# Kernel optimization log

Measured on AMD Instinct MI355X. Metric: run time of the kernel, lower is better.

The kernel has to match this reference:

```python
import jax, jax.numpy as jnp
import numpy as np

B = 65536
IN_F = 1024
OUT_F = 1024
N_ACT = 4  # len(activation_functions): tanh, sin, relu, sigmoid (cyclic over columns)


def setup_inputs() -> dict:
    key = jax.random.key(0)
    k1, k2 = jax.random.split(key)
    x = jax.random.normal(k1, (B, IN_F), dtype=jnp.float32)
    # xavier_uniform for weight [out, in]
    limit = float(np.sqrt(6.0 / (IN_F + OUT_F)))
    W = jax.random.uniform(k2, (OUT_F, IN_F), dtype=jnp.float32, minval=-limit, maxval=limit)
    b = jnp.zeros((OUT_F,), dtype=jnp.float32)
    return {"input": x, "W": W, "b": b}


def _apply_cyclic_acts(y):
    # column i gets activation (i % N_ACT); OUT_F % N_ACT == 0 so reshape to groups
    Bb, O = y.shape
    yg = y.reshape(Bb, O // N_ACT, N_ACT)
    out = jnp.stack([
        jnp.tanh(yg[..., 0]),
        jnp.sin(yg[..., 1]),
        jax.nn.relu(yg[..., 2]),
        jax.nn.sigmoid(yg[..., 3]),
    ], axis=-1)
    return out.reshape(Bb, O)


def reference(input, W, b) -> jnp.ndarray:
    y = jnp.einsum('bi,oi->bo', input, W) + b  # F.linear
    return _apply_cyclic_acts(y)
```

## Files before the change

### kernel.cpp

```cpp
#include <hip/hip_runtime.h>

constexpr int B_ROWS = 65536;
constexpr int IN_F   = 1024;
constexpr int OUT_F  = 1024;

constexpr int BDIM = 512;
constexpr int BM = 256, BN = 256, BK = 64;

typedef __bf16 bf16x8 __attribute__((ext_vector_type(8)));
typedef float  f32x4  __attribute__((ext_vector_type(4)));

__device__ __forceinline__ bf16x8 cvt8(f32x4 u0, f32x4 u1) {
    bf16x8 v;
    v[0] = (__bf16)u0[0]; v[1] = (__bf16)u0[1]; v[2] = (__bf16)u0[2]; v[3] = (__bf16)u0[3];
    v[4] = (__bf16)u1[0]; v[5] = (__bf16)u1[1]; v[6] = (__bf16)u1[2]; v[7] = (__bf16)u1[3];
    return v;
}

__device__ __forceinline__ void glds16(const __bf16* g, unsigned char* l) {
    __builtin_amdgcn_global_load_lds(
        (const __attribute__((address_space(1))) unsigned int*)(const void*)g,
        (__attribute__((address_space(3))) unsigned int*)(void*)l,
        16, 0, 0);
}

__global__ __launch_bounds__(256)
void w_to_bf16(const float* __restrict__ W, __bf16* __restrict__ Wb) {
    const size_t i = ((size_t)blockIdx.x * 256 + threadIdx.x) * 16;
    f32x4 a0 = *(const f32x4*)(W + i);
    f32x4 a1 = *(const f32x4*)(W + i + 4);
    f32x4 a2 = *(const f32x4*)(W + i + 8);
    f32x4 a3 = *(const f32x4*)(W + i + 12);
    *(bf16x8*)(Wb + i)     = cvt8(a0, a1);
    *(bf16x8*)(Wb + i + 8) = cvt8(a2, a3);
}

__global__ __launch_bounds__(BDIM, 2)
void fused_linear_act(const float* __restrict__ X,
                      const __bf16* __restrict__ Wb,
                      const float* __restrict__ bias,
                      float* __restrict__ O)
{
    __shared__ __attribute__((aligned(16))) unsigned char lds[2 * 65536];

    const int bx  = blockIdx.x;
    const int xcd = bx & 7;
    const int idx = bx >> 3;
    const int nt  = idx & 3;
    const int mt  = xcd + 8 * (idx >> 2);
    const int m0 = mt * BM;
    const int n0 = nt * BN;

    const int tid  = threadIdx.x;
    const int lane = tid & 63;
    const int wave = tid >> 6;
    const int wr2  = wave >> 2;
    const int w4   = wave & 3;
    const int lrow = lane & 15;
    const int quad = lane >> 4;

    const int arow = tid >> 1;
    const int ah   = tid & 1;
    const float* asrc = X + (size_t)(m0 + arow) * IN_F + ah * 32;
    const int awr = ah * 16384 + (arow >> 4) * 1024 + (arow & 15) * 16;

    const __bf16* bgp = Wb + (size_t)(n0 + 32 * wave + lrow) * IN_F + quad * 8;

    unsigned char* const b0 = lds;
    unsigned char* const b1 = lds + 65536;

    f32x4 acc[8][4];
    #pragma unroll
    for (int i = 0; i < 8; ++i)
        #pragma unroll
        for (int j = 0; j < 4; ++j)
            acc[i][j] = (f32x4){0.f, 0.f, 0.f, 0.f};

    f32x4 ar0, ar1, ar2, ar3, ar4, ar5, ar6, ar7;
    bf16x8 aq0, aq1, aq2, aq3, bq0, bq1, bq2, bq3;

#define ALOAD_LO(KA) do { \
    ar0 = *(const f32x4*)(asrc + (KA));      ar1 = *(const f32x4*)(asrc + (KA) + 4);  \
    ar2 = *(const f32x4*)(asrc + (KA) + 8);  ar3 = *(const f32x4*)(asrc + (KA) + 12); } while (0)
#define ALOAD_HI(KA) do { \
    ar4 = *(const f32x4*)(asrc + (KA) + 16); ar5 = *(const f32x4*)(asrc + (KA) + 20); \
    ar6 = *(const f32x4*)(asrc + (KA) + 24); ar7 = *(const f32x4*)(asrc + (KA) + 28); } while (0)
#define DSW(BUF) do { unsigned char* _w = (BUF) + awr; \
    *(bf16x8*)(_w)       = cvt8(ar0, ar1); \
    *(bf16x8*)(_w + 256) = cvt8(ar2, ar3); \
    *(bf16x8*)(_w + 512) = cvt8(ar4, ar5); \
    *(bf16x8*)(_w + 768) = cvt8(ar6, ar7); } while (0)
#define GBALL(BUF, K) do { unsigned char* _d0 = (BUF) + 32768 + wave * 2048; \
    unsigned char* _d1 = _d0 + 16384; \
    glds16(bgp + (K), _d0);      glds16(bgp + (K) + 16 * IN_F, _d0 + 1024); \
    glds16(bgp + (K) + 32, _d1); glds16(bgp + (K) + 32 + 16 * IN_F, _d1 + 1024); } while (0)
#define RA(BUF, KH, MH) do { \
    const unsigned char* _r = (BUF) + (KH) * 16384 + (wr2 * 8 + (MH) * 4) * 1024 + lane * 16; \
    aq0 = *(const bf16x8*)(_r);        aq1 = *(const bf16x8*)(_r + 1024); \
    aq2 = *(const bf16x8*)(_r + 2048); aq3 = *(const bf16x8*)(_r + 3072); } while (0)
#define RB(BUF, KH) do { \
    const unsigned char* _r = (BUF) + 32768 + (KH) * 16384 + (w4 * 4) * 1024 + lane * 16; \
    bq0 = *(const bf16x8*)(_r);        bq1 = *(const bf16x8*)(_r + 1024); \
    bq2 = *(const bf16x8*)(_r + 2048); bq3 = *(const bf16x8*)(_r + 3072); } while (0)
#define MFMA1(MH, I, J) acc[(MH)*4+(I)][(J)] = \
    __builtin_amdgcn_mfma_f32_16x16x32_bf16(aq##I, bq##J, acc[(MH)*4+(I)][(J)], 0, 0, 0)
#define MFMAQ(MH) do { __builtin_amdgcn_s_setprio(1); \
    MFMA1(MH,0,0); MFMA1(MH,0,1); MFMA1(MH,0,2); MFMA1(MH,0,3); \
    MFMA1(MH,1,0); MFMA1(MH,1,1); MFMA1(MH,1,2); MFMA1(MH,1,3); \
    MFMA1(MH,2,0); MFMA1(MH,2,1); MFMA1(MH,2,2); MFMA1(MH,2,3); \
    MFMA1(MH,3,0); MFMA1(MH,3,1); MFMA1(MH,3,2); MFMA1(MH,3,3); \
    __builtin_amdgcn_s_setprio(0); } while (0)
#define BAR() __builtin_amdgcn_s_barrier()
#define VM8() asm volatile("s_waitcnt vmcnt(8)" ::: "memory")
#define VM0() asm volatile("s_waitcnt vmcnt(0)" ::: "memory")
#define VMNONE() ((void)0)

#define ROUND(CUR, OPP, DO_STAGE, KB1, DO_ALOAD, KA2, VMW) do { \
     if (DO_STAGE) { GBALL(OPP, KB1); DSW(OPP); } \
             RB(CUR, 0); RA(CUR, 0, 0); BAR(); MFMAQ(0); BAR(); \
     if (DO_ALOAD) ALOAD_LO(KA2); \
             RA(CUR, 0, 1); BAR(); MFMAQ(1); BAR(); \
     if (DO_ALOAD) ALOAD_HI(KA2); \
             RB(CUR, 1); RA(CUR, 1, 0); BAR(); MFMAQ(0); BAR(); \
     RA(CUR, 1, 1); BAR(); MFMAQ(1); VMW(); BAR(); \
} while (0)

    ALOAD_LO(0); ALOAD_HI(0);
    GBALL(b0, 0);
    DSW(b0);
    ALOAD_LO(64); ALOAD_HI(64);
    asm volatile("s_waitcnt vmcnt(8) lgkmcnt(0)" ::: "memory");
    BAR();

    #pragma unroll 1
    for (int t = 0; t < 14; t += 2) {
        ROUND(b0, b1, true, (t + 1) * 64, true, (t + 2) * 64, VM8);
        ROUND(b1, b0, true, (t + 2) * 64, true, (t + 3) * 64, VM8);
    }
    ROUND(b0, b1, true, 15 * 64, false, 0, VM0);
    ROUND(b1, b0, false, 0, false, 0, VMNONE);

    const int s = lane & 3;
    const float kmul = (s == 0) ? -2.f : -1.f;
    const float aa   = (s == 0) ?  2.f :  1.f;
    const float cc   = (s == 0) ? -1.f :  0.f;
    const bool  is_sin  = (s == 1);
    const bool  is_relu = (s == 2);

    float bv[4];
    #pragma unroll
    for (int fn = 0; fn < 4; ++fn) bv[fn] = bias[n0 + w4 * 64 + fn * 16 + lrow];

    #pragma unroll
    for (int fm = 0; fm < 8; ++fm) {
        #pragma unroll
        for (int r = 0; r < 4; ++r) {
            const int gr = m0 + wr2 * 128 + fm * 16 + quad * 4 + r;
            float* op = O + (size_t)gr * OUT_F + n0 + w4 * 64 + lrow;
            #pragma unroll
            for (int fn = 0; fn < 4; ++fn) {
                const float y = acc[fm][fn][r] + bv[fn];
                const float e = __expf(kmul * y);
                const float g = fmaf(aa, __builtin_amdgcn_rcpf(1.f + e), cc);
                const float sv = __sinf(y);
                const float rv = fmaxf(y, 0.f);
                const float res = is_sin ? sv : (is_relu ? rv : g);
                op[fn * 16] = res;
            }
        }
    }
}

extern "C" void kernel_launch(void* const* d_in, const int* in_sizes, int n_in,
                              void* d_out, int out_size, void* d_ws, size_t ws_size,
                              hipStream_t stream) {
    const float* X = (const float*)d_in[0];
    const float* W = (const float*)d_in[1];
    const float* b = (const float*)d_in[2];
    float* O = (float*)d_out;
    __bf16* Wb = (__bf16*)d_ws;

    const size_t nW = (size_t)OUT_F * IN_F;
    w_to_bf16<<<(int)(nW / (256 * 16)), 256, 0, stream>>>(W, Wb);

    const int grid = (B_ROWS / BM) * (OUT_F / BN);
    fused_linear_act<<<grid, BDIM, 0, stream>>>(X, Wb, b, O);
}
```

Measured before the change: 613.8 us.

## Split batch between fused fp32-A kernel and pre-converted bf16 GEMM

The first half of the rows is processed by the fused kernel, which loads fp32 X and converts it in registers. This version issues the A loads all at once behind a sched barrier. The second half of X is first converted to bf16 by a separate kernel. That half then runs through a GEMM that streams both A and B via direct global-to-LDS loads, with finer-grained prefetch. The aim is to lower register and VALU pressure and improve load pipelining for part of the batch, at the cost of an extra pass over half of X and extra workspace. If the workspace is too small, the code falls back to the fused-only kernel.

```diff
diff --git a/kernel.cpp b/kernel.cpp
--- a/kernel.cpp
+++ b/kernel.cpp
@@ -35,65 +35,17 @@
     *(bf16x8*)(Wb + i + 8) = cvt8(a2, a3);
 }
 
-__global__ __launch_bounds__(BDIM, 2)
-void fused_linear_act(const float* __restrict__ X,
-                      const __bf16* __restrict__ Wb,
-                      const float* __restrict__ bias,
-                      float* __restrict__ O)
-{
-    __shared__ __attribute__((aligned(16))) unsigned char lds[2 * 65536];
-
-    const int bx  = blockIdx.x;
-    const int xcd = bx & 7;
-    const int idx = bx >> 3;
-    const int nt  = idx & 3;
-    const int mt  = xcd + 8 * (idx >> 2);
-    const int m0 = mt * BM;
-    const int n0 = nt * BN;
-
-    const int tid  = threadIdx.x;
-    const int lane = tid & 63;
-    const int wave = tid >> 6;
-    const int wr2  = wave >> 2;
-    const int w4   = wave & 3;
-    const int lrow = lane & 15;
-    const int quad = lane >> 4;
-
-    const int arow = tid >> 1;
-    const int ah   = tid & 1;
-    const float* asrc = X + (size_t)(m0 + arow) * IN_F + ah * 32;
-    const int awr = ah * 16384 + (arow >> 4) * 1024 + (arow & 15) * 16;
-
-    const __bf16* bgp = Wb + (size_t)(n0 + 32 * wave + lrow) * IN_F + quad * 8;
-
-    unsigned char* const b0 = lds;
-    unsigned char* const b1 = lds + 65536;
-
-    f32x4 acc[8][4];
-    #pragma unroll
-    for (int i = 0; i < 8; ++i)
-        #pragma unroll
-        for (int j = 0; j < 4; ++j)
-            acc[i][j] = (f32x4){0.f, 0.f, 0.f, 0.f};
-
-    f32x4 ar0, ar1, ar2, ar3, ar4, ar5, ar6, ar7;
-    bf16x8 aq0, aq1, aq2, aq3, bq0, bq1, bq2, bq3;
-
-#define ALOAD_LO(KA) do { \
-    ar0 = *(const f32x4*)(asrc + (KA));      ar1 = *(const f32x4*)(asrc + (KA) + 4);  \
-    ar2 = *(const f32x4*)(asrc + (KA) + 8);  ar3 = *(const f32x4*)(asrc + (KA) + 12); } while (0)
-#define ALOAD_HI(KA) do { \
-    ar4 = *(const f32x4*)(asrc + (KA) + 16); ar5 = *(const f32x4*)(asrc + (KA) + 20); \
-    ar6 = *(const f32x4*)(asrc + (KA) + 24); ar7 = *(const f32x4*)(asrc + (KA) + 28); } while (0)
-#define DSW(BUF) do { unsigned char* _w = (BUF) + awr; \
-    *(bf16x8*)(_w)       = cvt8(ar0, ar1); \
-    *(bf16x8*)(_w + 256) = cvt8(ar2, ar3); \
-    *(bf16x8*)(_w + 512) = cvt8(ar4, ar5); \
-    *(bf16x8*)(_w + 768) = cvt8(ar6, ar7); } while (0)
-#define GBALL(BUF, K) do { unsigned char* _d0 = (BUF) + 32768 + wave * 2048; \
-    unsigned char* _d1 = _d0 + 16384; \
-    glds16(bgp + (K), _d0);      glds16(bgp + (K) + 16 * IN_F, _d0 + 1024); \
-    glds16(bgp + (K) + 32, _d1); glds16(bgp + (K) + 32 + 16 * IN_F, _d1 + 1024); } while (0)
+__global__ __launch_bounds__(256)
+void cvt_half(const float* __restrict__ X, __bf16* __restrict__ Xb) {
+    const size_t i = (size_t)32768 * IN_F + ((size_t)blockIdx.x * 256 + threadIdx.x) * 16;
+    f32x4 a0 = *(const f32x4*)(X + i);
+    f32x4 a1 = *(const f32x4*)(X + i + 4);
+    f32x4 a2 = *(const f32x4*)(X + i + 8);
+    f32x4 a3 = *(const f32x4*)(X + i + 12);
+    *(bf16x8*)(Xb + i)     = cvt8(a0, a1);
+    *(bf16x8*)(Xb + i + 8) = cvt8(a2, a3);
+}
+
 #define RA(BUF, KH, MH) do { \
     const unsigned char* _r = (BUF) + (KH) * 16384 + (wr2 * 8 + (MH) * 4) * 1024 + lane * 16; \
     aq0 = *(const bf16x8*)(_r);        aq1 = *(const bf16x8*)(_r + 1024); \
@@ -112,17 +64,105 @@
     __builtin_amdgcn_s_setprio(0); } while (0)
 #define BAR() __builtin_amdgcn_s_barrier()
 #define VM8() asm volatile("s_waitcnt vmcnt(8)" ::: "memory")
+#define VM4() asm volatile("s_waitcnt vmcnt(4)" ::: "memory")
 #define VM0() asm volatile("s_waitcnt vmcnt(0)" ::: "memory")
 #define VMNONE() ((void)0)
 
-#define ROUND(CUR, OPP, DO_STAGE, KB1, DO_ALOAD, KA2, VMW) do { \
-     if (DO_STAGE) { GBALL(OPP, KB1); DSW(OPP); } \
-             RB(CUR, 0); RA(CUR, 0, 0); BAR(); MFMAQ(0); BAR(); \
-     if (DO_ALOAD) ALOAD_LO(KA2); \
-             RA(CUR, 0, 1); BAR(); MFMAQ(1); BAR(); \
-     if (DO_ALOAD) ALOAD_HI(KA2); \
-             RB(CUR, 1); RA(CUR, 1, 0); BAR(); MFMAQ(0); BAR(); \
-     RA(CUR, 1, 1); BAR(); MFMAQ(1); VMW(); BAR(); \
+#define EPILOGUE() do { \
+    const int s = lane & 3; \
+    const float kmul = (s == 0) ? -2.f : -1.f; \
+    const float aa   = (s == 0) ?  2.f :  1.f; \
+    const float cc   = (s == 0) ? -1.f :  0.f; \
+    const bool  is_sin  = (s == 1); \
+    const bool  is_relu = (s == 2); \
+    float bv[4]; \
+    _Pragma("unroll") \
+    for (int fn = 0; fn < 4; ++fn) bv[fn] = bias[n0 + w4 * 64 + fn * 16 + lrow]; \
+    _Pragma("unroll") \
+    for (int fm = 0; fm < 8; ++fm) { \
+        _Pragma("unroll") \
+        for (int r = 0; r < 4; ++r) { \
+            const int gr = m0 + wr2 * 128 + fm * 16 + quad * 4 + r; \
+            float* op = O + (size_t)gr * OUT_F + n0 + w4 * 64 + lrow; \
+            _Pragma("unroll") \
+            for (int fn = 0; fn < 4; ++fn) { \
+                const float y = acc[fm][fn][r] + bv[fn]; \
+                const float e = __expf(kmul * y); \
+                const float g = fmaf(aa, __builtin_amdgcn_rcpf(1.f + e), cc); \
+                const float sv = __sinf(y); \
+                const float rv = fmaxf(y, 0.f); \
+                const float res = is_sin ? sv : (is_relu ? rv : g); \
+                op[fn * 16] = res; \
+            } \
+        } \
+    } \
+} while (0)
+
+__global__ __launch_bounds__(BDIM, 2)
+void fused_v2(const float* __restrict__ X, const __bf16* __restrict__ Wb,
+              const float* __restrict__ bias, float* __restrict__ O, int m_base)
+{
+    __shared__ __attribute__((aligned(16))) unsigned char lds[2 * 65536];
+
+    const int bx  = blockIdx.x;
+    const int xcd = bx & 7;
+    const int idx = bx >> 3;
+    const int nt  = idx & 3;
+    const int mtl = xcd + 8 * (idx >> 2);
+    const int m0 = m_base + mtl * BM;
+    const int n0 = nt * BN;
+
+    const int tid  = threadIdx.x;
+    const int lane = tid & 63;
+    const int wave = tid >> 6;
+    const int wr2  = wave >> 2;
+    const int w4   = wave & 3;
+    const int lrow = lane & 15;
+    const int quad = lane >> 4;
+
+    const int arow = tid >> 1;
+    const int ah   = tid & 1;
+    const float* asrc = X + (size_t)(m0 + arow) * IN_F + ah * 32;
+    const int awr = ah * 16384 + (arow >> 4) * 1024 + (arow & 15) * 16;
+
+    const __bf16* bgp = Wb + (size_t)(n0 + 32 * wave + lrow) * IN_F + quad * 8;
+
+    unsigned char* const b0 = lds;
+    unsigned char* const b1 = lds + 65536;
+
+    f32x4 acc[8][4];
+    #pragma unroll
+    for (int i = 0; i < 8; ++i)
+        #pragma unroll
+        for (int j = 0; j < 4; ++j)
+            acc[i][j] = (f32x4){0.f, 0.f, 0.f, 0.f};
+
+    f32x4 ar0, ar1, ar2, ar3, ar4, ar5, ar6, ar7;
+    bf16x8 aq0, aq1, aq2, aq3, bq0, bq1, bq2, bq3;
+
+#define ALOAD_LO(KA) do { \
+    ar0 = *(const f32x4*)(asrc + (KA));      ar1 = *(const f32x4*)(asrc + (KA) + 4);  \
+    ar2 = *(const f32x4*)(asrc + (KA) + 8);  ar3 = *(const f32x4*)(asrc + (KA) + 12); } while (0)
+#define ALOAD_HI(KA) do { \
+    ar4 = *(const f32x4*)(asrc + (KA) + 16); ar5 = *(const f32x4*)(asrc + (KA) + 20); \
+    ar6 = *(const f32x4*)(asrc + (KA) + 24); ar7 = *(const f32x4*)(asrc + (KA) + 28); } while (0)
+#define DSW(BUF) do { unsigned char* _w = (BUF) + awr; \
+    *(bf16x8*)(_w)       = cvt8(ar0, ar1); \
+    *(bf16x8*)(_w + 256) = cvt8(ar2, ar3); \
+    *(bf16x8*)(_w + 512) = cvt8(ar4, ar5); \
+    *(bf16x8*)(_w + 768) = cvt8(ar6, ar7); } while (0)
+#define GBALL(BUF, K) do { unsigned char* _d0 = (BUF) + 32768 + wave * 2048; \
+    unsigned char* _d1 = _d0 + 16384; \
+    glds16(bgp + (K), _d0);      glds16(bgp + (K) + 16 * IN_F, _d0 + 1024); \
+    glds16(bgp + (K) + 32, _d1); glds16(bgp + (K) + 32 + 16 * IN_F, _d1 + 1024); } while (0)
+
+#define FROUND(CUR, OPP, DO_STAGE, KB1, DO_ALOAD, KA2, VMW) do { \
+    if (DO_STAGE) { GBALL(OPP, KB1); DSW(OPP); } \
+    if (DO_ALOAD) { ALOAD_LO(KA2); ALOAD_HI(KA2); __builtin_amdgcn_sched_barrier(0); } \
+    RB(CUR, 0); RA(CUR, 0, 0); BAR(); MFMAQ(0); BAR(); \
+    RA(CUR, 0, 1); BAR(); MFMAQ(1); BAR(); \
+    RB(CUR, 1); RA(CUR, 1, 0); BAR(); MFMAQ(0); BAR(); \
+    RA(CUR, 1, 1); BAR(); MFMAQ(1); VMW(); BAR(); \
 } while (0)
 
     ALOAD_LO(0); ALOAD_HI(0);
@@ -134,41 +174,96 @@
 
     #pragma unroll 1
     for (int t = 0; t < 14; t += 2) {
-        ROUND(b0, b1, true, (t + 1) * 64, true, (t + 2) * 64, VM8);
-        ROUND(b1, b0, true, (t + 2) * 64, true, (t + 3) * 64, VM8);
+        FROUND(b0, b1, true, (t + 1) * 64, true, (t + 2) * 64, VM8);
+        FROUND(b1, b0, true, (t + 2) * 64, true, (t + 3) * 64, VM8);
     }
-    ROUND(b0, b1, true, 15 * 64, false, 0, VM0);
-    ROUND(b1, b0, false, 0, false, 0, VMNONE);
-
-    const int s = lane & 3;
-    const float kmul = (s == 0) ? -2.f : -1.f;
-    const float aa   = (s == 0) ?  2.f :  1.f;
-    const float cc   = (s == 0) ? -1.f :  0.f;
-    const bool  is_sin  = (s == 1);
-    const bool  is_relu = (s == 2);
-
-    float bv[4];
+    FROUND(b0, b1, true, 15 * 64, false, 0, VM0);
+    FROUND(b1, b0, false, 0, false, 0, VMNONE);
+
+    EPILOGUE();
+#undef ALOAD_LO
+#undef ALOAD_HI
+#undef DSW
+#undef GBALL
+#undef FROUND
+}
+
+__global__ __launch_bounds__(BDIM, 2)
+void gemm_split(const __bf16* __restrict__ Xb, const __bf16* __restrict__ Wb,
+                const float* __restrict__ bias, float* __restrict__ O, int m_base)
+{
+    __shared__ __attribute__((aligned(16))) unsigned char lds[2 * 65536];
+
+    const int bx  = blockIdx.x;
+    const int xcd = bx & 7;
+    const int idx = bx >> 3;
+    const int nt  = idx & 3;
+    const int mtl = xcd + 8 * (idx >> 2);
+    const int m0 = m_base + mtl * BM;
+    const int n0 = nt * BN;
+
+    const int tid  = threadIdx.x;
+    const int lane = tid & 63;
+    const int wave = tid >> 6;
+    const int wr2  = wave >> 2;
+    const int w4   = wave & 3;
+    const int lrow = lane & 15;
+    const int quad = lane >> 4;
+
+    const __bf16* agp = Xb + (size_t)(m0 + 32 * wave + lrow) * IN_F + quad * 8;
+    const __bf16* bgp = Wb + (size_t)(n0 + 32 * wave + lrow) * IN_F + quad * 8;
+
+    unsigned char* const b0 = lds;
+    unsigned char* const b1 = lds + 65536;
+
+    f32x4 acc[8][4];
     #pragma unroll
-    for (int fn = 0; fn < 4; ++fn) bv[fn] = bias[n0 + w4 * 64 + fn * 16 + lrow];
-
-    #pragma unroll
-    for (int fm = 0; fm < 8; ++fm) {
+    for (int i = 0; i < 8; ++i)
         #pragma unroll
-        for (int r = 0; r < 4; ++r) {
-            const int gr = m0 + wr2 * 128 + fm * 16 + quad * 4 + r;
-            float* op = O + (size_t)gr * OUT_F + n0 + w4 * 64 + lrow;
-            #pragma unroll
-            for (int fn = 0; fn < 4; ++fn) {
-                const float y = acc[fm][fn][r] + bv[fn];
-                const float e = __expf(kmul * y);
-                const float g = fmaf(aa, __builtin_amdgcn_rcpf(1.f + e), cc);
-                const float sv = __sinf(y);
-                const float rv = fmaxf(y, 0.f);
-                const float res = is_sin ? sv : (is_relu ? rv : g);
-                op[fn * 16] = res;
-            }
-        }
+        for (int j = 0; j < 4; ++j)
+            acc[i][j] = (f32x4){0.f, 0.f, 0.f, 0.f};
+
+    bf16x8 aq0, aq1, aq2, aq3, bq0, bq1, bq2, bq3;
+
+#define GA(BUF, KH, K) do { unsigned char* _d = (BUF) + (KH) * 16384 + wave * 2048; \
+    glds16(agp + (K), _d); glds16(agp + (K) + 16 * IN_F, _d + 1024); } while (0)
+#define GB(BUF, KH, K) do { unsigned char* _d = (BUF) + 32768 + (KH) * 16384 + wave * 2048; \
+    glds16(bgp + (K), _d); glds16(bgp + (K) + 16 * IN_F, _d + 1024); } while (0)
+#define SROUND(CUR, OPP, KT) do { \
+    GA(OPP, 1, ((KT) + 1) * 64 + 32); RB(CUR, 0); RA(CUR, 0, 0); \
+             BAR(); MFMAQ(0); BAR(); \
+    GB(OPP, 1, ((KT) + 1) * 64 + 32); RA(CUR, 0, 1); \
+             BAR(); MFMAQ(1); BAR(); \
+    GA(CUR, 0, ((KT) + 2) * 64); RB(CUR, 1); RA(CUR, 1, 0); \
+             BAR(); MFMAQ(0); BAR(); \
+    GB(CUR, 0, ((KT) + 2) * 64); RA(CUR, 1, 1); \
+             BAR(); MFMAQ(1); VM4(); BAR(); \
+} while (0)
+
+    GA(b0, 0, 0);  GB(b0, 0, 0);
+    GA(b0, 1, 32); GB(b0, 1, 32);
+    GA(b1, 0, 64); GB(b1, 0, 64);
+    VM4();
+    BAR();
+
+    #pragma unroll 1
+    for (int kt = 0; kt < 14; kt += 2) {
+        SROUND(b0, b1, kt);
+        SROUND(b1, b0, kt + 1);
     }
+    GA(b1, 1, 15 * 64 + 32); RB(b0, 0); RA(b0, 0, 0); BAR(); MFMAQ(0); BAR();
+    GB(b1, 1, 15 * 64 + 32); RA(b0, 0, 1);            BAR(); MFMAQ(1); BAR();
+    RB(b0, 1); RA(b0, 1, 0);                          BAR(); MFMAQ(0); BAR();
+    RA(b0, 1, 1);                                     BAR(); MFMAQ(1); VM0(); BAR();
+    RB(b1, 0); RA(b1, 0, 0); BAR(); MFMAQ(0); BAR();
+    RA(b1, 0, 1);            BAR(); MFMAQ(1); BAR();
+    RB(b1, 1); RA(b1, 1, 0); BAR(); MFMAQ(0); BAR();
+    RA(b1, 1, 1);            BAR(); MFMAQ(1);
+
+    EPILOGUE();
+#undef GA
+#undef GB
+#undef SROUND
 }
 
 extern "C" void kernel_launch(void* const* d_in, const int* in_sizes, int n_in,
@@ -178,11 +273,19 @@
     const float* W = (const float*)d_in[1];
     const float* b = (const float*)d_in[2];
     float* O = (float*)d_out;
+
+    const size_t nX = (size_t)B_ROWS * IN_F;
+    const size_t nW = (size_t)OUT_F * IN_F;
     __bf16* Wb = (__bf16*)d_ws;
-
-    const size_t nW = (size_t)OUT_F * IN_F;
+    __bf16* Xb = (__bf16*)d_ws + nW;
+
     w_to_bf16<<<(int)(nW / (256 * 16)), 256, 0, stream>>>(W, Wb);
 
-    const int grid = (B_ROWS / BM) * (OUT_F / BN);
-    fused_linear_act<<<grid, BDIM, 0, stream>>>(X, Wb, b, O);
-}
+    if (ws_size >= (nW + nX) * sizeof(__bf16)) {
+        fused_v2<<<512, BDIM, 0, stream>>>(X, Wb, b, O, 0);
+        cvt_half<<<(int)((nX / 2) / (256 * 16)), 256, 0, stream>>>(X, Xb);
+        gemm_split<<<512, BDIM, 0, stream>>>(Xb, Wb, b, O, 32768);
+    } else {
+        fused_v2<<<1024, BDIM, 0, stream>>>(X, Wb, b, O, 0);
+    }
+}
```

After: 590.7 us. 3.8% less time.

## Load fp32 X tiles directly to LDS with triple-buffered BK=32 pipeline

Applied to the files above, without the earlier changes.

X tiles now go straight to LDS in fp32 through global_load_lds instead of passing through registers and being converted before the LDS write. Conversion to bf16 moves to the LDS read side. K tile drops to 32 with three LDS buffers, so global loads for stage k+2 overlap compute on stage k. The wave layout changes from 2x4 to 4x2 to cut redundant A conversions. The cost is more barriers per K, since there are twice as many rounds, plus extra conversion work and fp32 LDS read traffic for A.

```diff
diff --git a/kernel.cpp b/kernel.cpp
--- a/kernel.cpp
+++ b/kernel.cpp
@@ -5,7 +5,7 @@
 constexpr int OUT_F  = 1024;
 
 constexpr int BDIM = 512;
-constexpr int BM = 256, BN = 256, BK = 64;
+constexpr int BM = 256, BN = 256, BK = 32;
 
 typedef __bf16 bf16x8 __attribute__((ext_vector_type(8)));
 typedef float  f32x4  __attribute__((ext_vector_type(4)));
@@ -17,9 +17,9 @@
     return v;
 }
 
-__device__ __forceinline__ void glds16(const __bf16* g, unsigned char* l) {
+__device__ __forceinline__ void glds16(const void* g, unsigned char* l) {
     __builtin_amdgcn_global_load_lds(
-        (const __attribute__((address_space(1))) unsigned int*)(const void*)g,
+        (const __attribute__((address_space(1))) unsigned int*)g,
         (__attribute__((address_space(3))) unsigned int*)(void*)l,
         16, 0, 0);
 }
@@ -41,7 +41,7 @@
                       const float* __restrict__ bias,
                       float* __restrict__ O)
 {
-    __shared__ __attribute__((aligned(16))) unsigned char lds[2 * 65536];
+    __shared__ __attribute__((aligned(16))) unsigned char lds[3 * 49152];
 
     const int bx  = blockIdx.x;
     const int xcd = bx & 7;
@@ -54,91 +54,82 @@
     const int tid  = threadIdx.x;
     const int lane = tid & 63;
     const int wave = tid >> 6;
-    const int wr2  = wave >> 2;
-    const int w4   = wave & 3;
+    const int wr4  = wave >> 1;
+    const int wn2  = wave & 1;
     const int lrow = lane & 15;
     const int quad = lane >> 4;
 
-    const int arow = tid >> 1;
-    const int ah   = tid & 1;
-    const float* asrc = X + (size_t)(m0 + arow) * IN_F + ah * 32;
-    const int awr = ah * 16384 + (arow >> 4) * 1024 + (arow & 15) * 16;
-
-    const __bf16* bgp = Wb + (size_t)(n0 + 32 * wave + lrow) * IN_F + quad * 8;
+    const float*  agp = X  + (size_t)(m0 + lrow) * IN_F + quad * 4;
+    const __bf16* bgp = Wb + (size_t)(n0 + lrow) * IN_F + quad * 8;
+    const int bi0 = 2 * wave, bi1 = 2 * wave + 1;
+    const int ci0 = 2 * wave, ci1 = 2 * wave + 1;
 
     unsigned char* const b0 = lds;
-    unsigned char* const b1 = lds + 65536;
+    unsigned char* const b1 = lds + 49152;
+    unsigned char* const b2 = lds + 98304;
 
-    f32x4 acc[8][4];
+    f32x4 acc[4][8];
     #pragma unroll
-    for (int i = 0; i < 8; ++i)
+    for (int i = 0; i < 4; ++i)
         #pragma unroll
-        for (int j = 0; j < 4; ++j)
+        for (int j = 0; j < 8; ++j)
             acc[i][j] = (f32x4){0.f, 0.f, 0.f, 0.f};
 
-    f32x4 ar0, ar1, ar2, ar3, ar4, ar5, ar6, ar7;
     bf16x8 aq0, aq1, aq2, aq3, bq0, bq1, bq2, bq3;
 
-#define ALOAD_LO(KA) do { \
-    ar0 = *(const f32x4*)(asrc + (KA));      ar1 = *(const f32x4*)(asrc + (KA) + 4);  \
-    ar2 = *(const f32x4*)(asrc + (KA) + 8);  ar3 = *(const f32x4*)(asrc + (KA) + 12); } while (0)
-#define ALOAD_HI(KA) do { \
-    ar4 = *(const f32x4*)(asrc + (KA) + 16); ar5 = *(const f32x4*)(asrc + (KA) + 20); \
-    ar6 = *(const f32x4*)(asrc + (KA) + 24); ar7 = *(const f32x4*)(asrc + (KA) + 28); } while (0)
-#define DSW(BUF) do { unsigned char* _w = (BUF) + awr; \
-    *(bf16x8*)(_w)       = cvt8(ar0, ar1); \
-    *(bf16x8*)(_w + 256) = cvt8(ar2, ar3); \
-    *(bf16x8*)(_w + 512) = cvt8(ar4, ar5); \
-    *(bf16x8*)(_w + 768) = cvt8(ar6, ar7); } while (0)
-#define GBALL(BUF, K) do { unsigned char* _d0 = (BUF) + 32768 + wave * 2048; \
-    unsigned char* _d1 = _d0 + 16384; \
-    glds16(bgp + (K), _d0);      glds16(bgp + (K) + 16 * IN_F, _d0 + 1024); \
-    glds16(bgp + (K) + 32, _d1); glds16(bgp + (K) + 32 + 16 * IN_F, _d1 + 1024); } while (0)
-#define RA(BUF, KH, MH) do { \
-    const unsigned char* _r = (BUF) + (KH) * 16384 + (wr2 * 8 + (MH) * 4) * 1024 + lane * 16; \
-    aq0 = *(const bf16x8*)(_r);        aq1 = *(const bf16x8*)(_r + 1024); \
-    aq2 = *(const bf16x8*)(_r + 2048); aq3 = *(const bf16x8*)(_r + 3072); } while (0)
-#define RB(BUF, KH) do { \
-    const unsigned char* _r = (BUF) + 32768 + (KH) * 16384 + (w4 * 4) * 1024 + lane * 16; \
+#define GA(BUF, BI, G, K) \
+    glds16(agp + (size_t)(BI) * 16384 + (G) * 16 + (K), (BUF) + (BI) * 2048 + (G) * 1024)
+#define GB(BUF, CI, K) \
+    glds16(bgp + (size_t)(CI) * 16384 + (K), (BUF) + 32768 + (CI) * 1024)
+#define RAALL(BUF) do { \
+    const unsigned char* _p = (BUF) + (wr4 * 4) * 2048 + quad * 512 + lrow * 16; \
+    f32x4 _h0, _h1; \
+    _h0 = *(const f32x4*)(_p);        _h1 = *(const f32x4*)(_p + 256);        aq0 = cvt8(_h0, _h1); \
+    _h0 = *(const f32x4*)(_p + 2048); _h1 = *(const f32x4*)(_p + 2048 + 256); aq1 = cvt8(_h0, _h1); \
+    _h0 = *(const f32x4*)(_p + 4096); _h1 = *(const f32x4*)(_p + 4096 + 256); aq2 = cvt8(_h0, _h1); \
+    _h0 = *(const f32x4*)(_p + 6144); _h1 = *(const f32x4*)(_p + 6144 + 256); aq3 = cvt8(_h0, _h1); \
+} while (0)
+#define RBH(BUF, NH) do { \
+    const unsigned char* _r = (BUF) + 32768 + (wn2 * 8 + (NH) * 4) * 1024 + lane * 16; \
     bq0 = *(const bf16x8*)(_r);        bq1 = *(const bf16x8*)(_r + 1024); \
     bq2 = *(const bf16x8*)(_r + 2048); bq3 = *(const bf16x8*)(_r + 3072); } while (0)
-#define MFMA1(MH, I, J) acc[(MH)*4+(I)][(J)] = \
-    __builtin_amdgcn_mfma_f32_16x16x32_bf16(aq##I, bq##J, acc[(MH)*4+(I)][(J)], 0, 0, 0)
-#define MFMAQ(MH) do { __builtin_amdgcn_s_setprio(1); \
-    MFMA1(MH,0,0); MFMA1(MH,0,1); MFMA1(MH,0,2); MFMA1(MH,0,3); \
-    MFMA1(MH,1,0); MFMA1(MH,1,1); MFMA1(MH,1,2); MFMA1(MH,1,3); \
-    MFMA1(MH,2,0); MFMA1(MH,2,1); MFMA1(MH,2,2); MFMA1(MH,2,3); \
-    MFMA1(MH,3,0); MFMA1(MH,3,1); MFMA1(MH,3,2); MFMA1(MH,3,3); \
+#define MFMA1(NH, I, J) acc[(I)][(NH)*4+(J)] = \
+    __builtin_amdgcn_mfma_f32_16x16x32_bf16(aq##I, bq##J, acc[(I)][(NH)*4+(J)], 0, 0, 0)
+#define MFMAQ(NH) do { __builtin_amdgcn_s_setprio(1); \
+    MFMA1(NH,0,0); MFMA1(NH,0,1); MFMA1(NH,0,2); MFMA1(NH,0,3); \
+    MFMA1(NH,1,0); MFMA1(NH,1,1); MFMA1(NH,1,2); MFMA1(NH,1,3); \
+    MFMA1(NH,2,0); MFMA1(NH,2,1); MFMA1(NH,2,2); MFMA1(NH,2,3); \
+    MFMA1(NH,3,0); MFMA1(NH,3,1); MFMA1(NH,3,2); MFMA1(NH,3,3); \
     __builtin_amdgcn_s_setprio(0); } while (0)
 #define BAR() __builtin_amdgcn_s_barrier()
-#define VM8() asm volatile("s_waitcnt vmcnt(8)" ::: "memory")
+#define VM6() asm volatile("s_waitcnt vmcnt(6)" ::: "memory")
 #define VM0() asm volatile("s_waitcnt vmcnt(0)" ::: "memory")
 #define VMNONE() ((void)0)
 
-#define ROUND(CUR, OPP, DO_STAGE, KB1, DO_ALOAD, KA2, VMW) do { \
-     if (DO_STAGE) { GBALL(OPP, KB1); DSW(OPP); } \
-             RB(CUR, 0); RA(CUR, 0, 0); BAR(); MFMAQ(0); BAR(); \
-     if (DO_ALOAD) ALOAD_LO(KA2); \
-             RA(CUR, 0, 1); BAR(); MFMAQ(1); BAR(); \
-     if (DO_ALOAD) ALOAD_HI(KA2); \
-             RB(CUR, 1); RA(CUR, 1, 0); BAR(); MFMAQ(0); BAR(); \
-     RA(CUR, 1, 1); BAR(); MFMAQ(1); VMW(); BAR(); \
+#define RND(CUR, NXT, DO_G, KT2, VMW) do { \
+     if (DO_G) { GA(NXT, bi0, 0, KT2); GA(NXT, bi0, 1, KT2); GB(NXT, ci0, KT2); } \
+             RAALL(CUR); RBH(CUR, 0); \
+             BAR(); MFMAQ(0); BAR(); \
+     if (DO_G) { GA(NXT, bi1, 0, KT2); GA(NXT, bi1, 1, KT2); GB(NXT, ci1, KT2); } \
+             RBH(CUR, 1); \
+             BAR(); MFMAQ(1); VMW(); BAR(); \
 } while (0)
 
-    ALOAD_LO(0); ALOAD_HI(0);
-    GBALL(b0, 0);
-    DSW(b0);
-    ALOAD_LO(64); ALOAD_HI(64);
-    asm volatile("s_waitcnt vmcnt(8) lgkmcnt(0)" ::: "memory");
+    GA(b0, bi0, 0, 0);  GA(b0, bi0, 1, 0);  GB(b0, ci0, 0);
+    GA(b0, bi1, 0, 0);  GA(b0, bi1, 1, 0);  GB(b0, ci1, 0);
+    GA(b1, bi0, 0, 32); GA(b1, bi0, 1, 32); GB(b1, ci0, 32);
+    GA(b1, bi1, 0, 32); GA(b1, bi1, 1, 32); GB(b1, ci1, 32);
+    VM6();
     BAR();
 
     #pragma unroll 1
-    for (int t = 0; t < 14; t += 2) {
-        ROUND(b0, b1, true, (t + 1) * 64, true, (t + 2) * 64, VM8);
-        ROUND(b1, b0, true, (t + 2) * 64, true, (t + 3) * 64, VM8);
+    for (int r = 0; r < 30; r += 3) {
+        RND(b0, b2, true, (r + 2) * 32, VM6);
+        RND(b1, b0, true, (r + 3) * 32, VM6);
+        RND(b2, b1, true, (r + 4) * 32, VM6);
     }
-    ROUND(b0, b1, true, 15 * 64, false, 0, VM0);
-    ROUND(b1, b0, false, 0, false, 0, VMNONE);
+    RND(b0, b1, false, 0, VM0);
+    RND(b1, b0, false, 0, VMNONE);
 
     const int s = lane & 3;
     const float kmul = (s == 0) ? -2.f : -1.f;
@@ -147,18 +138,18 @@
     const bool  is_sin  = (s == 1);
     const bool  is_relu = (s == 2);
 
-    float bv[4];
+    float bv[8];
     #pragma unroll
-    for (int fn = 0; fn < 4; ++fn) bv[fn] = bias[n0 + w4 * 64 + fn * 16 + lrow];
+    for (int fn = 0; fn < 8; ++fn) bv[fn] = bias[n0 + wn2 * 128 + fn * 16 + lrow];
 
     #pragma unroll
-    for (int fm = 0; fm < 8; ++fm) {
+    for (int fm = 0; fm < 4; ++fm) {
         #pragma unroll
         for (int r = 0; r < 4; ++r) {
-            const int gr = m0 + wr2 * 128 + fm * 16 + quad * 4 + r;
-            float* op = O + (size_t)gr * OUT_F + n0 + w4 * 64 + lrow;
+            const int gr = m0 + wr4 * 64 + fm * 16 + quad * 4 + r;
+            float* op = O + (size_t)gr * OUT_F + n0 + wn2 * 128 + lrow;
             #pragma unroll
-            for (int fn = 0; fn < 4; ++fn) {
+            for (int fn = 0; fn < 8; ++fn) {
                 const float y = acc[fm][fn][r] + bv[fn];
                 const float e = __expf(kmul * y);
                 const float g = fmaf(aa, __builtin_amdgcn_rcpf(1.f + e), cc);
```

Result: faster. 590.4 us (-3.8%).

## Pre-convert X to bf16 and use persistent direct-to-LDS GEMM

Applied to the files above, without the earlier changes.

Adds a pre-pass that converts the whole input X to bf16 in workspace, together with W. The GEMM then loads both operands straight into LDS with global_load_lds instead of loading fp32 into registers and converting. The GEMM becomes persistent: 256 blocks each process four M tiles, with the prologue of the next tile overlapped with the tail of the current one, and outputs are written with nontemporal stores. The cost is an extra full read and write pass over X (about 256MB read and 128MB written), in exchange for halving the bytes the GEMM reads for A and removing conversion work from the main loop. A fallback path is kept for when the workspace is too small.

```diff
diff --git a/kernel.cpp b/kernel.cpp
--- a/kernel.cpp
+++ b/kernel.cpp
@@ -25,31 +25,45 @@
 }
 
 __global__ __launch_bounds__(256)
-void w_to_bf16(const float* __restrict__ W, __bf16* __restrict__ Wb) {
-    const size_t i = ((size_t)blockIdx.x * 256 + threadIdx.x) * 16;
-    f32x4 a0 = *(const f32x4*)(W + i);
-    f32x4 a1 = *(const f32x4*)(W + i + 4);
-    f32x4 a2 = *(const f32x4*)(W + i + 8);
-    f32x4 a3 = *(const f32x4*)(W + i + 12);
-    *(bf16x8*)(Wb + i)     = cvt8(a0, a1);
-    *(bf16x8*)(Wb + i + 8) = cvt8(a2, a3);
+void cvt_all(const float* __restrict__ X, const float* __restrict__ W,
+             __bf16* __restrict__ Xb, __bf16* __restrict__ Wb) {
+    const int b = blockIdx.x;
+    if (b < 2048) {
+        size_t i = ((size_t)b * 256 + threadIdx.x) * 16;
+        #pragma unroll 1
+        for (int it = 0; it < 8; ++it, i += (size_t)2048 * 256 * 16) {
+            f32x4 a0 = __builtin_nontemporal_load((const f32x4*)(X + i));
+            f32x4 a1 = __builtin_nontemporal_load((const f32x4*)(X + i + 4));
+            f32x4 a2 = __builtin_nontemporal_load((const f32x4*)(X + i + 8));
+            f32x4 a3 = __builtin_nontemporal_load((const f32x4*)(X + i + 12));
+            *(bf16x8*)(Xb + i)     = cvt8(a0, a1);
+            *(bf16x8*)(Xb + i + 8) = cvt8(a2, a3);
+        }
+    } else {
+        const size_t i = ((size_t)(b - 2048) * 256 + threadIdx.x) * 16;
+        f32x4 a0 = __builtin_nontemporal_load((const f32x4*)(W + i));
+        f32x4 a1 = __builtin_nontemporal_load((const f32x4*)(W + i + 4));
+        f32x4 a2 = __builtin_nontemporal_load((const f32x4*)(W + i + 8));
+        f32x4 a3 = __builtin_nontemporal_load((const f32x4*)(W + i + 12));
+        *(bf16x8*)(Wb + i)     = cvt8(a0, a1);
+        *(bf16x8*)(Wb + i + 8) = cvt8(a2, a3);
+    }
 }
 
 __global__ __launch_bounds__(BDIM, 2)
-void fused_linear_act(const float* __restrict__ X,
-                      const __bf16* __restrict__ Wb,
-                      const float* __restrict__ bias,
-                      float* __restrict__ O)
+void gemm4(const __bf16* __restrict__ Xb,
+           const __bf16* __restrict__ Wb,
+           const float* __restrict__ bias,
+           float* __restrict__ O)
 {
     __shared__ __attribute__((aligned(16))) unsigned char lds[2 * 65536];
 
-    const int bx  = blockIdx.x;
-    const int xcd = bx & 7;
-    const int idx = bx >> 3;
-    const int nt  = idx & 3;
-    const int mt  = xcd + 8 * (idx >> 2);
-    const int m0 = mt * BM;
-    const int n0 = nt * BN;
+    const int bx   = blockIdx.x;
+    const int xcd  = bx & 7;
+    const int slot = bx >> 3;
+    const int nq   = slot & 3;
+    const int g    = xcd + 8 * (slot >> 2);
+    const int n0   = nq * BN;
 
     const int tid  = threadIdx.x;
     const int lane = tid & 63;
@@ -59,41 +73,20 @@
     const int lrow = lane & 15;
     const int quad = lane >> 4;
 
-    const int arow = tid >> 1;
-    const int ah   = tid & 1;
-    const float* asrc = X + (size_t)(m0 + arow) * IN_F + ah * 32;
-    const int awr = ah * 16384 + (arow >> 4) * 1024 + (arow & 15) * 16;
-
+    const size_t arowoff = (size_t)(32 * wave + lrow) * IN_F + quad * 8;
+    const __bf16* agp = Xb + (size_t)(g * 256) * IN_F + arowoff;
     const __bf16* bgp = Wb + (size_t)(n0 + 32 * wave + lrow) * IN_F + quad * 8;
 
     unsigned char* const b0 = lds;
     unsigned char* const b1 = lds + 65536;
 
     f32x4 acc[8][4];
-    #pragma unroll
-    for (int i = 0; i < 8; ++i)
-        #pragma unroll
-        for (int j = 0; j < 4; ++j)
-            acc[i][j] = (f32x4){0.f, 0.f, 0.f, 0.f};
-
-    f32x4 ar0, ar1, ar2, ar3, ar4, ar5, ar6, ar7;
     bf16x8 aq0, aq1, aq2, aq3, bq0, bq1, bq2, bq3;
 
-#define ALOAD_LO(KA) do { \
-    ar0 = *(const f32x4*)(asrc + (KA));      ar1 = *(const f32x4*)(asrc + (KA) + 4);  \
-    ar2 = *(const f32x4*)(asrc + (KA) + 8);  ar3 = *(const f32x4*)(asrc + (KA) + 12); } while (0)
-#define ALOAD_HI(KA) do { \
-    ar4 = *(const f32x4*)(asrc + (KA) + 16); ar5 = *(const f32x4*)(asrc + (KA) + 20); \
-    ar6 = *(const f32x4*)(asrc + (KA) + 24); ar7 = *(const f32x4*)(asrc + (KA) + 28); } while (0)
-#define DSW(BUF) do { unsigned char* _w = (BUF) + awr; \
-    *(bf16x8*)(_w)       = cvt8(ar0, ar1); \
-    *(bf16x8*)(_w + 256) = cvt8(ar2, ar3); \
-    *(bf16x8*)(_w + 512) = cvt8(ar4, ar5); \
-    *(bf16x8*)(_w + 768) = cvt8(ar6, ar7); } while (0)
-#define GBALL(BUF, K) do { unsigned char* _d0 = (BUF) + 32768 + wave * 2048; \
-    unsigned char* _d1 = _d0 + 16384; \
-    glds16(bgp + (K), _d0);      glds16(bgp + (K) + 16 * IN_F, _d0 + 1024); \
-    glds16(bgp + (K) + 32, _d1); glds16(bgp + (K) + 32 + 16 * IN_F, _d1 + 1024); } while (0)
+#define GA(P, BUF, KH, K) do { unsigned char* _d = (BUF) + (KH) * 16384 + wave * 2048; \
+    glds16((P) + (K), _d); glds16((P) + (K) + 16 * IN_F, _d + 1024); } while (0)
+#define GB(BUF, KH, K) do { unsigned char* _d = (BUF) + 32768 + (KH) * 16384 + wave * 2048; \
+    glds16(bgp + (K), _d); glds16(bgp + (K) + 16 * IN_F, _d + 1024); } while (0)
 #define RA(BUF, KH, MH) do { \
     const unsigned char* _r = (BUF) + (KH) * 16384 + (wr2 * 8 + (MH) * 4) * 1024 + lane * 16; \
     aq0 = *(const bf16x8*)(_r);        aq1 = *(const bf16x8*)(_r + 1024); \
@@ -111,34 +104,19 @@
     MFMA1(MH,3,0); MFMA1(MH,3,1); MFMA1(MH,3,2); MFMA1(MH,3,3); \
     __builtin_amdgcn_s_setprio(0); } while (0)
 #define BAR() __builtin_amdgcn_s_barrier()
-#define VM8() asm volatile("s_waitcnt vmcnt(8)" ::: "memory")
+#define VM4() asm volatile("s_waitcnt vmcnt(4)" ::: "memory")
 #define VM0() asm volatile("s_waitcnt vmcnt(0)" ::: "memory")
-#define VMNONE() ((void)0)
-
-#define ROUND(CUR, OPP, DO_STAGE, KB1, DO_ALOAD, KA2, VMW) do { \
-     if (DO_STAGE) { GBALL(OPP, KB1); DSW(OPP); } \
-             RB(CUR, 0); RA(CUR, 0, 0); BAR(); MFMAQ(0); BAR(); \
-     if (DO_ALOAD) ALOAD_LO(KA2); \
-             RA(CUR, 0, 1); BAR(); MFMAQ(1); BAR(); \
-     if (DO_ALOAD) ALOAD_HI(KA2); \
-             RB(CUR, 1); RA(CUR, 1, 0); BAR(); MFMAQ(0); BAR(); \
-     RA(CUR, 1, 1); BAR(); MFMAQ(1); VMW(); BAR(); \
+
+#define SROUND(P, CUR, OPP, KT) do { \
+    GA(P, OPP, 1, ((KT) + 1) * 64 + 32); RB(CUR, 0); RA(CUR, 0, 0); \
+             BAR(); MFMAQ(0); BAR(); \
+    GB(OPP, 1, ((KT) + 1) * 64 + 32); RA(CUR, 0, 1); \
+             BAR(); MFMAQ(1); BAR(); \
+    GA(P, CUR, 0, ((KT) + 2) * 64); RB(CUR, 1); RA(CUR, 1, 0); \
+             BAR(); MFMAQ(0); BAR(); \
+    GB(CUR, 0, ((KT) + 2) * 64); RA(CUR, 1, 1); \
+             BAR(); MFMAQ(1); VM4(); BAR(); \
 } while (0)
-
-    ALOAD_LO(0); ALOAD_HI(0);
-    GBALL(b0, 0);
-    DSW(b0);
-    ALOAD_LO(64); ALOAD_HI(64);
-    asm volatile("s_waitcnt vmcnt(8) lgkmcnt(0)" ::: "memory");
-    BAR();
-
-    #pragma unroll 1
-    for (int t = 0; t < 14; t += 2) {
-        ROUND(b0, b1, true, (t + 1) * 64, true, (t + 2) * 64, VM8);
-        ROUND(b1, b0, true, (t + 2) * 64, true, (t + 3) * 64, VM8);
-    }
-    ROUND(b0, b1, true, 15 * 64, false, 0, VM0);
-    ROUND(b1, b0, false, 0, false, 0, VMNONE);
 
     const int s = lane & 3;
     const float kmul = (s == 0) ? -2.f : -1.f;
@@ -146,11 +124,165 @@
     const float cc   = (s == 0) ? -1.f :  0.f;
     const bool  is_sin  = (s == 1);
     const bool  is_relu = (s == 2);
-
     float bv[4];
     #pragma unroll
     for (int fn = 0; fn < 4; ++fn) bv[fn] = bias[n0 + w4 * 64 + fn * 16 + lrow];
 
+    #pragma unroll 1
+    for (int t = 0; t < 4; ++t) {
+        const bool more = (t < 3);
+        const __bf16* agpN = agp + (size_t)16384 * IN_F;
+        const int m0 = (g + 64 * t) * 256;
+
+        #pragma unroll
+        for (int i = 0; i < 8; ++i)
+            #pragma unroll
+            for (int j = 0; j < 4; ++j)
+                acc[i][j] = (f32x4){0.f, 0.f, 0.f, 0.f};
+
+        if (t == 0) {
+            GA(agp, b0, 0, 0);  GB(b0, 0, 0);
+            GA(agp, b0, 1, 32); GB(b0, 1, 32);
+            GA(agp, b1, 0, 64); GB(b1, 0, 64);
+            VM4();
+            BAR();
+        }
+        #pragma unroll 1
+        for (int kt = 0; kt < 14; kt += 2) {
+            SROUND(agp, b0, b1, kt);
+            SROUND(agp, b1, b0, kt + 1);
+        }
+        if (more) {
+            GA(agp, b1, 1, 15 * 64 + 32); RB(b0, 0); RA(b0, 0, 0); BAR(); MFMAQ(0); BAR();
+            GB(b1, 1, 15 * 64 + 32);      RA(b0, 0, 1);            BAR(); MFMAQ(1); BAR();
+            GA(agpN, b0, 0, 0);           RB(b0, 1); RA(b0, 1, 0); BAR(); MFMAQ(0); BAR();
+            GB(b0, 0, 0);                 RA(b0, 1, 1);            BAR(); MFMAQ(1); VM4(); BAR();
+            GA(agpN, b0, 1, 32);          RB(b1, 0); RA(b1, 0, 0); BAR(); MFMAQ(0); BAR();
+            GB(b0, 1, 32);                RA(b1, 0, 1);            BAR(); MFMAQ(1); BAR();
+            GA(agpN, b1, 0, 64);          RB(b1, 1); RA(b1, 1, 0); BAR(); MFMAQ(0); BAR();
+            GB(b1, 0, 64);                RA(b1, 1, 1);            BAR(); MFMAQ(1); VM4(); BAR();
+        } else {
+            GA(agp, b1, 1, 15 * 64 + 32); RB(b0, 0); RA(b0, 0, 0); BAR(); MFMAQ(0); BAR();
+            GB(b1, 1, 15 * 64 + 32);      RA(b0, 0, 1);            BAR(); MFMAQ(1); BAR();
+            RB(b0, 1); RA(b0, 1, 0);                               BAR(); MFMAQ(0); BAR();
+            RA(b0, 1, 1);                                          BAR(); MFMAQ(1); VM0(); BAR();
+            RB(b1, 0); RA(b1, 0, 0); BAR(); MFMAQ(0); BAR();
+            RA(b1, 0, 1);            BAR(); MFMAQ(1); BAR();
+            RB(b1, 1); RA(b1, 1, 0); BAR(); MFMAQ(0); BAR();
+            RA(b1, 1, 1);            BAR(); MFMAQ(1); BAR();
+        }
+
+        #pragma unroll
+        for (int fm = 0; fm < 8; ++fm) {
+            #pragma unroll
+            for (int r = 0; r < 4; ++r) {
+                const int gr = m0 + wr2 * 128 + fm * 16 + quad * 4 + r;
+                float* op = O + (size_t)gr * OUT_F + n0 + w4 * 64 + lrow;
+                #pragma unroll
+                for (int fn = 0; fn < 4; ++fn) {
+                    const float y = acc[fm][fn][r] + bv[fn];
+                    const float e = __expf(kmul * y);
+                    const float gg = fmaf(aa, __builtin_amdgcn_rcpf(1.f + e), cc);
+                    const float sv = __sinf(y);
+                    const float rv = fmaxf(y, 0.f);
+                    const float res = is_sin ? sv : (is_relu ? rv : gg);
+                    __builtin_nontemporal_store(res, op + fn * 16);
+                }
+            }
+        }
+        agp = agpN;
+    }
+}
+
+__global__ __launch_bounds__(256)
+void w_to_bf16(const float* __restrict__ W, __bf16* __restrict__ Wb) {
+    const size_t i = ((size_t)blockIdx.x * 256 + threadIdx.x) * 16;
+    f32x4 a0 = *(const f32x4*)(W + i);
+    f32x4 a1 = *(const f32x4*)(W + i + 4);
+    f32x4 a2 = *(const f32x4*)(W + i + 8);
+    f32x4 a3 = *(const f32x4*)(W + i + 12);
+    *(bf16x8*)(Wb + i)     = cvt8(a0, a1);
+    *(bf16x8*)(Wb + i + 8) = cvt8(a2, a3);
+}
+
+__global__ __launch_bounds__(BDIM, 2)
+void fused_fallback(const float* __restrict__ X, const __bf16* __restrict__ Wb,
+                    const float* __restrict__ bias, float* __restrict__ O)
+{
+    __shared__ __attribute__((aligned(16))) unsigned char lds[2 * 65536];
+    const int bx  = blockIdx.x;
+    const int xcd = bx & 7;
+    const int idx = bx >> 3;
+    const int nt  = idx & 3;
+    const int mt  = xcd + 8 * (idx >> 2);
+    const int m0 = mt * BM;
+    const int n0 = nt * BN;
+    const int tid  = threadIdx.x;
+    const int lane = tid & 63;
+    const int wave = tid >> 6;
+    const int wr2  = wave >> 2;
+    const int w4   = wave & 3;
+    const int lrow = lane & 15;
+    const int quad = lane >> 4;
+    const int arow = tid >> 1;
+    const int ah   = tid & 1;
+    const float* asrc = X + (size_t)(m0 + arow) * IN_F + ah * 32;
+    const int awr = ah * 16384 + (arow >> 4) * 1024 + (arow & 15) * 16;
+    const __bf16* bgp = Wb + (size_t)(n0 + 32 * wave + lrow) * IN_F + quad * 8;
+    unsigned char* const b0 = lds;
+    unsigned char* const b1 = lds + 65536;
+    f32x4 acc[8][4];
+    #pragma unroll
+    for (int i = 0; i < 8; ++i)
+        #pragma unroll
+        for (int j = 0; j < 4; ++j)
+            acc[i][j] = (f32x4){0.f, 0.f, 0.f, 0.f};
+    f32x4 ar0, ar1, ar2, ar3, ar4, ar5, ar6, ar7;
+    bf16x8 aq0, aq1, aq2, aq3, bq0, bq1, bq2, bq3;
+#define ALOAD(KA) do { \
+    ar0 = *(const f32x4*)(asrc + (KA));      ar1 = *(const f32x4*)(asrc + (KA) + 4);  \
+    ar2 = *(const f32x4*)(asrc + (KA) + 8);  ar3 = *(const f32x4*)(asrc + (KA) + 12); \
+    ar4 = *(const f32x4*)(asrc + (KA) + 16); ar5 = *(const f32x4*)(asrc + (KA) + 20); \
+    ar6 = *(const f32x4*)(asrc + (KA) + 24); ar7 = *(const f32x4*)(asrc + (KA) + 28); } while (0)
+#define DSW(BUF) do { unsigned char* _w = (BUF) + awr; \
+    *(bf16x8*)(_w)       = cvt8(ar0, ar1); \
+    *(bf16x8*)(_w + 256) = cvt8(ar2, ar3); \
+    *(bf16x8*)(_w + 512) = cvt8(ar4, ar5); \
+    *(bf16x8*)(_w + 768) = cvt8(ar6, ar7); } while (0)
+#define GBALL(BUF, K) do { unsigned char* _d0 = (BUF) + 32768 + wave * 2048; \
+    unsigned char* _d1 = _d0 + 16384; \
+    glds16(bgp + (K), _d0);      glds16(bgp + (K) + 16 * IN_F, _d0 + 1024); \
+    glds16(bgp + (K) + 32, _d1); glds16(bgp + (K) + 32 + 16 * IN_F, _d1 + 1024); } while (0)
+#define FROUND(CUR, OPP, DO_STAGE, KB1, DO_ALOAD, KA2, VMW) do { \
+    if (DO_STAGE) { GBALL(OPP, KB1); DSW(OPP); } \
+    if (DO_ALOAD) { ALOAD(KA2); __builtin_amdgcn_sched_barrier(0); } \
+    RB(CUR, 0); RA(CUR, 0, 0); BAR(); MFMAQ(0); BAR(); \
+    RA(CUR, 0, 1); BAR(); MFMAQ(1); BAR(); \
+    RB(CUR, 1); RA(CUR, 1, 0); BAR(); MFMAQ(0); BAR(); \
+    RA(CUR, 1, 1); BAR(); MFMAQ(1); VMW; BAR(); \
+} while (0)
+    ALOAD(0);
+    GBALL(b0, 0);
+    DSW(b0);
+    ALOAD(64);
+    asm volatile("s_waitcnt vmcnt(8) lgkmcnt(0)" ::: "memory");
+    BAR();
+    #pragma unroll 1
+    for (int t = 0; t < 14; t += 2) {
+        FROUND(b0, b1, true, (t + 1) * 64, true, (t + 2) * 64, asm volatile("s_waitcnt vmcnt(8)" ::: "memory"));
+        FROUND(b1, b0, true, (t + 2) * 64, true, (t + 3) * 64, asm volatile("s_waitcnt vmcnt(8)" ::: "memory"));
+    }
+    FROUND(b0, b1, true, 15 * 64, false, 0, VM0());
+    FROUND(b1, b0, false, 0, false, 0, (void)0);
+    const int s = lane & 3;
+    const float kmul = (s == 0) ? -2.f : -1.f;
+    const float aa   = (s == 0) ?  2.f :  1.f;
+    const float cc   = (s == 0) ? -1.f :  0.f;
+    const bool  is_sin  = (s == 1);
+    const bool  is_relu = (s == 2);
+    float bv[4];
+    #pragma unroll
+    for (int fn = 0; fn < 4; ++fn) bv[fn] = bias[n0 + w4 * 64 + fn * 16 + lrow];
     #pragma unroll
     for (int fm = 0; fm < 8; ++fm) {
         #pragma unroll
@@ -161,10 +293,10 @@
             for (int fn = 0; fn < 4; ++fn) {
                 const float y = acc[fm][fn][r] + bv[fn];
                 const float e = __expf(kmul * y);
-                const float g = fmaf(aa, __builtin_amdgcn_rcpf(1.f + e), cc);
+                const float gg = fmaf(aa, __builtin_amdgcn_rcpf(1.f + e), cc);
                 const float sv = __sinf(y);
                 const float rv = fmaxf(y, 0.f);
-                const float res = is_sin ? sv : (is_relu ? rv : g);
+                const float res = is_sin ? sv : (is_relu ? rv : gg);
                 op[fn * 16] = res;
             }
         }
@@ -178,11 +310,18 @@
     const float* W = (const float*)d_in[1];
     const float* b = (const float*)d_in[2];
     float* O = (float*)d_out;
-    __bf16* Wb = (__bf16*)d_ws;
-
+
+    const size_t nX = (size_t)B_ROWS * IN_F;
     const size_t nW = (size_t)OUT_F * IN_F;
-    w_to_bf16<<<(int)(nW / (256 * 16)), 256, 0, stream>>>(W, Wb);
-
-    const int grid = (B_ROWS / BM) * (OUT_F / BN);
-    fused_linear_act<<<grid, BDIM, 0, stream>>>(X, Wb, b, O);
-}
+
+    if (ws_size >= (nW + nX) * sizeof(__bf16)) {
+        __bf16* Wb = (__bf16*)d_ws;
+        __bf16* Xb = (__bf16*)d_ws + nW;
+        cvt_all<<<2048 + 256, 256, 0, stream>>>(X, W, Xb, Wb);
+        gemm4<<<256, BDIM, 0, stream>>>(Xb, Wb, b, O);
+    } else {
+        __bf16* Wb = (__bf16*)d_ws;
+        w_to_bf16<<<(int)(nW / (256 * 16)), 256, 0, stream>>>(W, Wb);
+        fused_fallback<<<1024, BDIM, 0, stream>>>(X, Wb, b, O);
+    }
+}
```

Result: slower. 748.1 us (+21.9%).
